# Performance work log

Measured on AMD Instinct MI355X. Metric: run time of the kernel, lower is better.

Reference implementation:

```python
import jax, jax.numpy as jnp
import numpy as np

PRIME = 2147483647  # 2^31 - 1, MinHash modulus
GAMMA = 0.3
NUM_HEADS = 8


def minhash_sketch(ids, a, b):
    # ids: (B, L, S) int64 atom ids; a,b: (K,) hash coefficients
    # h[b,l,s,k] = (a[k]*id + b[k]) mod PRIME ; signature = min over the set axis S
    h = (ids[..., None] * a + b) % PRIME          # (B, L, S, K)
    return h.min(axis=2)                          # (B, L, K)


def jaccard_from_signatures(sig_q, sig_k):
    # sig_q: (B, Lq, K), sig_k: (B, Lk, K) -> (B, Lq, Lk) fraction of matching slots.
    # Scan over the K hash slots to avoid materializing a (B,Lq,Lk,K) tensor.
    B, Lq, K = sig_q.shape
    Lk = sig_k.shape[1]

    def step(acc, cols):
        qc, kc = cols                              # (B,Lq), (B,Lk)
        return acc + (qc[:, :, None] == kc[:, None, :]).astype(jnp.float32), None

    init = jnp.zeros((B, Lq, Lk), jnp.float32)
    xs = (jnp.moveaxis(sig_q, -1, 0), jnp.moveaxis(sig_k, -1, 0))
    acc, _ = jax.lax.scan(step, init, xs)
    return acc / K


def symdiff_from_jaccard(jacc, size_q, size_k):
    # |A ∩ B| = J/(1+J) * (|A|+|B|)  =>  |A Δ B| = (|A|+|B|) * (1-J)/(1+J)
    tot = size_q[:, :, None] + size_k[:, None, :]   # (B, Lq, Lk)
    return tot * (1.0 - jacc) / (1.0 + jacc)


def setup_inputs() -> dict:
    key = jax.random.key(0)
    ks = jax.random.split(key, 12)
    B, Lq, Lk, E, S, K, V = 4, 1024, 1024, 512, 8, 128, 32000
    w = lambda k: (jax.random.normal(k, (E, E), jnp.float32) * 0.02)
    return {
        "query": jax.random.normal(ks[0], (B, Lq, E), jnp.float32),
        "key": jax.random.normal(ks[1], (B, Lk, E), jnp.float32),
        "value": jax.random.normal(ks[2], (B, Lk, E), jnp.float32),
        "token_sets_q": jax.random.randint(ks[3], (B, Lq, S), 0, V).astype(jnp.int64),
        "token_sets_k": jax.random.randint(ks[4], (B, Lk, S), 0, V).astype(jnp.int64),
        "hash_a": jax.random.randint(ks[5], (K,), 1, PRIME - 1).astype(jnp.int64),
        "hash_b": jax.random.randint(ks[6], (K,), 0, PRIME - 1).astype(jnp.int64),
        "Wq": w(ks[7]), "bq": jnp.zeros((E,), jnp.float32),
        "Wk": w(ks[8]), "bk": jnp.zeros((E,), jnp.float32),
        "Wv": w(ks[9]), "bv": jnp.zeros((E,), jnp.float32),
        "Wo": w(ks[10]), "bo": jnp.zeros((E,), jnp.float32),
    }


def reference(query, key, value, token_sets_q, token_sets_k, hash_a, hash_b,
              Wq, bq, Wk, bk, Wv, bv, Wo, bo):
    B, Lq, E = query.shape
    Lk = key.shape[1]
    H = NUM_HEADS
    d = E // H

    # in-projections (torch Linear: x @ W^T + b); q,k are computed but the
    # attention scores come solely from the token-set kernel (gating disabled)
    q = query @ Wq.T + bq
    k = key @ Wk.T + bk
    v = (value @ Wv.T + bv).reshape(B, Lk, H, d).transpose(0, 2, 1, 3)  # (B,H,Lk,d)

    # MinHash sketches of per-token atom sets -> estimated Jaccard -> Δ-RBF score
    sig_q = minhash_sketch(token_sets_q, hash_a, hash_b)   # (B,Lq,K)
    sig_k = minhash_sketch(token_sets_k, hash_a, hash_b)   # (B,Lk,K)
    jacc = jaccard_from_signatures(sig_q, sig_k)           # (B,Lq,Lk)

    S = token_sets_q.shape[-1]
    size_q = jnp.full((B, Lq), S, jnp.float32)             # uniform CSR offsets -> |set| = S
    size_k = jnp.full((B, Lk), S, jnp.float32)
    delta = symdiff_from_jaccard(jacc, size_q, size_k)
    scores = jnp.exp(-GAMMA * delta)                       # (B,Lq,Lk), shared by all heads

    attn = jax.nn.softmax(scores, axis=-1)                 # no masks, no causal, dropout=0
    ctx = jnp.einsum('bqk,bhkd->bqhd', attn, v).reshape(B, Lq, E)
    return ctx @ Wo.T + bo
```

## Files before the change

### kernel.cpp

```cpp
#include <hip/hip_runtime.h>
#include <hip/hip_bf16.h>
#include <stdint.h>

#define PRIME 2147483647u
#define GAMMA 0.3f
#define K_HASH 128
#define S_SET 8
#define NB 4
#define LQ 1024
#define LK 1024
#define EDIM 512

typedef unsigned short ushort_t;
typedef __attribute__((ext_vector_type(8))) short short8;
typedef __attribute__((ext_vector_type(4))) float f32x4;

static __device__ __forceinline__ unsigned short f2bf(float f) {
    unsigned u = __builtin_bit_cast(unsigned, f);
    u += 0x7FFFu + ((u >> 16) & 1u);
    return (unsigned short)(u >> 16);
}

static __device__ __forceinline__ void glds16(const void* g, void* l) {
    __builtin_amdgcn_global_load_lds(
        (const __attribute__((address_space(1))) unsigned int*)g,
        (__attribute__((address_space(3))) unsigned int*)l, 16, 0, 0);
}

#define SWZ(r) ((((r) >> 2) & 3) ^ ((r) & 3))

static __device__ __forceinline__ unsigned nm2(unsigned acc, unsigned a,
                                               unsigned b, unsigned ones) {
    unsigned x = a ^ b, t;
    asm("v_pk_min_u16 %0, %1, %2" : "=v"(t) : "v"(x), "v"(ones));
    return acc + t;
}
static __device__ __forceinline__ unsigned nm8(unsigned acc, int4 q, int4 k,
                                               unsigned ones) {
    acc = nm2(acc, (unsigned)q.x, (unsigned)k.x, ones);
    acc = nm2(acc, (unsigned)q.y, (unsigned)k.y, ones);
    acc = nm2(acc, (unsigned)q.z, (unsigned)k.z, ones);
    acc = nm2(acc, (unsigned)q.w, (unsigned)k.w, ones);
    return acc;
}

#define CVT_N0 (NB * LK * EDIM)
#define CVT_N1 (EDIM * EDIM)
#define CVT_N2 (EDIM * EDIM)
__global__ __launch_bounds__(256) void cvt_kernel(
        const float* __restrict__ v, const float* __restrict__ wv,
        const float* __restrict__ wo,
        ushort_t* __restrict__ vb, ushort_t* __restrict__ wvb,
        ushort_t* __restrict__ wob) {
    size_t i = ((size_t)blockIdx.x * 256 + threadIdx.x) * 8;
    const float* src; ushort_t* dst; size_t off;
    if (i < CVT_N0)                { src = v;  dst = vb;  off = i; }
    else if (i < CVT_N0 + CVT_N1)  { src = wv; dst = wvb; off = i - CVT_N0; }
    else                           { src = wo; dst = wob; off = i - CVT_N0 - CVT_N1; }
    float4 a = *(const float4*)(src + off);
    float4 b = *(const float4*)(src + off + 4);
    ushort4 o0, o1;
    o0.x = f2bf(a.x); o0.y = f2bf(a.y); o0.z = f2bf(a.z); o0.w = f2bf(a.w);
    o1.x = f2bf(b.x); o1.y = f2bf(b.y); o1.z = f2bf(b.z); o1.w = f2bf(b.w);
    *(ushort4*)(dst + off)     = o0;
    *(ushort4*)(dst + off + 4) = o1;
}

__global__ __launch_bounds__(128) void sig_kernel(
        const int* __restrict__ ts_q, const int* __restrict__ ts_k,
        const int* __restrict__ ha, const int* __restrict__ hb,
        ushort_t* __restrict__ sig_q, ushort_t* __restrict__ sig_k,
        float* __restrict__ rs) {
    int blk = blockIdx.x;
    int k = threadIdx.x;
    if (blk < 32) rs[blk * 128 + k] = 0.f;
    const int* ts = (blk < NB * LQ) ? ts_q : ts_k;
    ushort_t* sig = (blk < NB * LQ) ? sig_q : sig_k;
    int idx = blk & (NB * LQ - 1);
    unsigned long long a  = (unsigned)ha[k];
    unsigned long long bb = (unsigned)hb[k];
    __shared__ int ids[S_SET];
    if (k < S_SET) ids[k] = ts[idx * S_SET + k];
    __syncthreads();
    unsigned mn = 0xFFFFFFFFu;
    #pragma unroll
    for (int s = 0; s < S_SET; s++) {
        unsigned long long x = a * (unsigned long long)(unsigned)ids[s] + bb;
        x = (x & PRIME) + (x >> 31);
        x = (x & PRIME) + (x >> 31);
        unsigned r = (unsigned)x;
        if (r >= PRIME) r -= PRIME;
        mn = (r < mn) ? r : mn;
    }
    sig[idx * K_HASH + k] = (ushort_t)mn;
}

__global__ __launch_bounds__(256) void jaccard_kernel(
        const ushort_t* __restrict__ sig_q, const ushort_t* __restrict__ sig_k,
        ushort_t* __restrict__ P, float* __restrict__ rs) {
    __shared__ int Qs[4][128 * 16];
    __shared__ int Ks[4][64 * 17];
    __shared__ float lut[K_HASH + 1];
    int tid = threadIdx.x;
    if (tid <= K_HASH) {
        float r = (float)(K_HASH - tid) / (float)(K_HASH + tid);
        lut[tid] = expf(expf(-GAMMA * (2.0f * S_SET) * r));
    }
    int b = blockIdx.z;
    int q0 = blockIdx.y * 128, j0 = blockIdx.x * 64;
    const int4* gq = (const int4*)(sig_q + ((size_t)b * LQ + q0) * K_HASH);
    const int4* gk = (const int4*)(sig_k + ((size_t)b * LK + j0) * K_HASH);
    int r0 = tid >> 2, g0 = tid & 3;
    int r1 = 64 + r0;
    #pragma unroll
    for (int ch = 0; ch < 4; ch++) {
        *(int4*)&Qs[ch][r0 * 16 + ((g0 + (r0 >> 3)) & 3) * 4] = gq[r0 * 16 + ch * 4 + g0];
        *(int4*)&Qs[ch][r1 * 16 + ((g0 + (r1 >> 3)) & 3) * 4] = gq[r1 * 16 + ch * 4 + g0];
        *(int4*)&Ks[ch][r0 * 17 + ((g0 + (r0 >> 5)) & 3) * 4] = gk[r0 * 16 + ch * 4 + g0];
    }
    __syncthreads();
    int tx = tid & 15, ty = tid >> 4;
    unsigned ones = 0x00010001u;
    unsigned acc[8][4] = {};
    #pragma unroll 1
    for (int ch = 0; ch < 4; ch++) {
        #pragma unroll
        for (int cc = 0; cc < 4; cc++) {
            int4 qv[8], kv[4];
            #pragma unroll
            for (int i = 0; i < 8; i++)
                qv[i] = *(const int4*)&Qs[ch][(ty * 8 + i) * 16 + ((cc + ty) & 3) * 4];
            #pragma unroll
            for (int j = 0; j < 4; j++)
                kv[j] = *(const int4*)&Ks[ch][(tx * 4 + j) * 17 + ((cc + (tx >> 3)) & 3) * 4];
            #pragma unroll
            for (int i = 0; i < 8; i++)
                #pragma unroll
                for (int j = 0; j < 4; j++)
                    acc[i][j] = nm8(acc[i][j], qv[i], kv[j], ones);
        }
    }
    ushort_t* Pb = P + (size_t)b * LQ * LK;
    float fsum[8];
    #pragma unroll
    for (int i = 0; i < 8; i++) {
        ushort4 o;
        unsigned nm0 = (acc[i][0] & 0xFFFFu) + (acc[i][0] >> 16);
        unsigned nm1 = (acc[i][1] & 0xFFFFu) + (acc[i][1] >> 16);
        unsigned nm2_ = (acc[i][2] & 0xFFFFu) + (acc[i][2] >> 16);
        unsigned nm3 = (acc[i][3] & 0xFFFFu) + (acc[i][3] >> 16);
        float p0 = lut[K_HASH - nm0], p1 = lut[K_HASH - nm1];
        float p2 = lut[K_HASH - nm2_], p3 = lut[K_HASH - nm3];
        fsum[i] = (p0 + p1) + (p2 + p3);
        o.x = f2bf(p0); o.y = f2bf(p1); o.z = f2bf(p2); o.w = f2bf(p3);
        int row = q0 + ty * 8 + i;
        *(ushort4*)&Pb[(size_t)row * LK + j0 + tx * 4] = o;
    }
    __syncthreads();
    float* fs = (float*)&Qs[0][0];
    #pragma unroll
    for (int i = 0; i < 8; i++) fs[(ty * 8 + i) * 16 + tx] = fsum[i];
    __syncthreads();
    if (tid < 128) {
        float s = 0.f;
        #pragma unroll
        for (int t = 0; t < 16; t++) s += fs[tid * 16 + t];
        atomicAdd(&rs[(size_t)b * LQ + q0 + tid], s);
    }
}

#define EPI_ROWBIAS  0
#define EPI_ROWDIV   1
#define EPI_COLBIAS  2

template<int OUTF32, int MODE>
__global__ __launch_bounds__(256) void btgemm_kernel(
        const ushort_t* __restrict__ A, const ushort_t* __restrict__ B,
        void* __restrict__ C,
        const float* __restrict__ bias, const float* __restrict__ scale,
        int lda, int ldb, int ldc, int Kd,
        long long sA, long long sB, long long sC, long long sS) {
    __shared__ ushort_t As[2][64 * 32];
    __shared__ ushort_t Bs[2][64 * 32];
    int z = blockIdx.z;
    int m0 = blockIdx.y * 64, n0 = blockIdx.x * 64;
    int tid = threadIdx.x;
    int w = tid >> 6, lane = tid & 63;
    int wm = (w & 1) * 32, wn = (w >> 1) * 32;
    int mrow = lane & 15, kg = lane >> 4;

    int r = tid >> 2, c = (tid & 3) ^ SWZ(r);
    const ushort_t* pa = A + (size_t)z * sA + (size_t)(m0 + r) * lda + c * 8;
    const ushort_t* pb = B + (size_t)z * sB + (size_t)(n0 + r) * ldb + c * 8;

    int aoff[2], boff[2];
    #pragma unroll
    for (int s = 0; s < 2; s++) {
        int Ra = wm + s * 16 + mrow;
        aoff[s] = Ra * 32 + (kg ^ SWZ(Ra)) * 8;
        int Rb = wn + s * 16 + mrow;
        boff[s] = Rb * 32 + (kg ^ SWZ(Rb)) * 8;
    }

    f32x4 acc[2][2] = {};
    int nK = Kd >> 5;
    glds16(pa, &As[0][tid * 8]);
    glds16(pb, &Bs[0][tid * 8]);
    for (int i = 0; i < nK; i++) {
        __syncthreads();
        int cur = i & 1, nxt = cur ^ 1;
        if (i + 1 < nK) {
            int k0 = (i + 1) << 5;
            glds16(pa + k0, &As[nxt][tid * 8]);
            glds16(pb + k0, &Bs[nxt][tid * 8]);
        }
        short8 af[2], bh[2];
        #pragma unroll
        for (int s = 0; s < 2; s++) {
            af[s] = *(const short8*)&As[cur][aoff[s]];
            bh[s] = *(const short8*)&Bs[cur][boff[s]];
        }
        #pragma unroll
        for (int ii = 0; ii < 2; ii++)
            #pragma unroll
            for (int jj = 0; jj < 2; jj++)
                acc[ii][jj] = __builtin_amdgcn_mfma_f32_16x16x32_bf16(
                                  af[ii], bh[jj], acc[ii][jj], 0, 0, 0);
    }

    const float* sc = scale + (size_t)z * sS;
    int col = lane & 15, rbase = (lane >> 4) * 4;
    #pragma unroll
    for (int ii = 0; ii < 2; ii++) {
        #pragma unroll
        for (int jj = 0; jj < 2; jj++) {
            #pragma unroll
            for (int rr = 0; rr < 4; rr++) {
                int gm = m0 + wm + ii * 16 + rbase + rr;
                int gn = n0 + wn + jj * 16 + col;
                float v = acc[ii][jj][rr];
                if (MODE == EPI_ROWBIAS)     v += bias[gm];
                else if (MODE == EPI_ROWDIV) v /= sc[gm];
                else                         v += bias[gn];
                size_t cix = (size_t)z * sC + (size_t)gm * ldc + gn;
                if (OUTF32) ((float*)C)[cix] = v;
                else        ((ushort_t*)C)[cix] = f2bf(v);
            }
        }
    }
}

extern "C" void kernel_launch(void* const* d_in, const int* in_sizes, int n_in,
                              void* d_out, int out_size, void* d_ws, size_t ws_size,
                              hipStream_t stream) {
    const float* value = (const float*)d_in[2];
    const int* tsq = (const int*)d_in[3];
    const int* tsk = (const int*)d_in[4];
    const int* ha  = (const int*)d_in[5];
    const int* hb  = (const int*)d_in[6];
    const float* Wv = (const float*)d_in[11];
    const float* bv = (const float*)d_in[12];
    const float* Wo = (const float*)d_in[13];
    const float* bo = (const float*)d_in[14];
    float* out = (float*)d_out;

    char* ws = (char*)d_ws;
    ushort_t* sigq   = (ushort_t*)(ws);
    ushort_t* sigk   = (ushort_t*)(ws + (1ull << 20));
    ushort_t* P      = (ushort_t*)(ws + (4ull << 20));
    float* rs        = (float*)(ws + (12ull << 20));
    ushort_t* Vt     = (ushort_t*)(ws + (12ull << 20) + (1ull << 16));
    ushort_t* ctx    = (ushort_t*)(ws + (17ull << 20));
    ushort_t* Vb     = (ushort_t*)(ws + (21ull << 20));
    ushort_t* Wvb    = (ushort_t*)(ws + (25ull << 20));
    ushort_t* Wob    = (ushort_t*)(ws + (25ull << 20) + (512ull << 10));

    cvt_kernel<<<(CVT_N0 + CVT_N1 + CVT_N2) / (256 * 8), 256, 0, stream>>>(
        value, Wv, Wo, Vb, Wvb, Wob);

    sig_kernel<<<2 * NB * LQ, 128, 0, stream>>>(tsq, tsk, ha, hb, sigq, sigk, rs);

    jaccard_kernel<<<dim3(LK / 64, LQ / 128, NB), 256, 0, stream>>>(sigq, sigk, P, rs);

    btgemm_kernel<0, EPI_ROWBIAS><<<dim3(4096 / 64, 512 / 64, 1), 256, 0, stream>>>(
        Wvb, Vb, Vt, bv, rs ,
        EDIM, EDIM, NB * LK, EDIM, 0LL, 0LL, 0LL, 0LL);

    btgemm_kernel<0, EPI_ROWDIV><<<dim3(EDIM / 64, LQ / 64, NB), 256, 0, stream>>>(
        P, Vt, ctx, bv , rs,
        LK, NB * LK, EDIM, LK,
        (long long)LQ * LK, (long long)LK, (long long)LQ * EDIM, (long long)LQ);

    btgemm_kernel<1, EPI_COLBIAS><<<dim3(EDIM / 64, NB * LQ / 64, 1), 256, 0, stream>>>(
        ctx, Wob, out, bo, rs ,
        EDIM, EDIM, EDIM, EDIM, 0LL, 0LL, 0LL, 0LL);
}
```

Baseline: 156.6 us.

## Fold Wv into Wo, merge prep kernels, fuse jaccard with weight GEMM

Precomputes W2 = Wo·Wv and bias2 = Wo·bv + bo, so the value projection GEMM over all tokens is removed. The remaining pipeline is P·V followed by ctx2·W2^T, with the row division and bias folded into the final epilogue. The bf16 conversion, transpose, signature hashing and bias setup are merged into one prep kernel, and the small weight GEMM runs as extra blocks inside the jaccard kernel, whose tile shrinks to 64x64. This cuts the launch count from six to four and removes a large GEMM, at the cost of a different rounding path (bf16 W2 and unprojected V).

```diff
diff --git a/kernel.cpp b/kernel.cpp
--- a/kernel.cpp
+++ b/kernel.cpp
@@ -44,154 +44,25 @@
     return acc;
 }
 
-#define CVT_N0 (NB * LK * EDIM)
-#define CVT_N1 (EDIM * EDIM)
-#define CVT_N2 (EDIM * EDIM)
-__global__ __launch_bounds__(256) void cvt_kernel(
-        const float* __restrict__ v, const float* __restrict__ wv,
-        const float* __restrict__ wo,
-        ushort_t* __restrict__ vb, ushort_t* __restrict__ wvb,
-        ushort_t* __restrict__ wob) {
-    size_t i = ((size_t)blockIdx.x * 256 + threadIdx.x) * 8;
-    const float* src; ushort_t* dst; size_t off;
-    if (i < CVT_N0)                { src = v;  dst = vb;  off = i; }
-    else if (i < CVT_N0 + CVT_N1)  { src = wv; dst = wvb; off = i - CVT_N0; }
-    else                           { src = wo; dst = wob; off = i - CVT_N0 - CVT_N1; }
-    float4 a = *(const float4*)(src + off);
-    float4 b = *(const float4*)(src + off + 4);
-    ushort4 o0, o1;
-    o0.x = f2bf(a.x); o0.y = f2bf(a.y); o0.z = f2bf(a.z); o0.w = f2bf(a.w);
-    o1.x = f2bf(b.x); o1.y = f2bf(b.y); o1.z = f2bf(b.z); o1.w = f2bf(b.w);
-    *(ushort4*)(dst + off)     = o0;
-    *(ushort4*)(dst + off + 4) = o1;
-}
-
-__global__ __launch_bounds__(128) void sig_kernel(
-        const int* __restrict__ ts_q, const int* __restrict__ ts_k,
-        const int* __restrict__ ha, const int* __restrict__ hb,
-        ushort_t* __restrict__ sig_q, ushort_t* __restrict__ sig_k,
-        float* __restrict__ rs) {
-    int blk = blockIdx.x;
-    int k = threadIdx.x;
-    if (blk < 32) rs[blk * 128 + k] = 0.f;
-    const int* ts = (blk < NB * LQ) ? ts_q : ts_k;
-    ushort_t* sig = (blk < NB * LQ) ? sig_q : sig_k;
-    int idx = blk & (NB * LQ - 1);
-    unsigned long long a  = (unsigned)ha[k];
-    unsigned long long bb = (unsigned)hb[k];
-    __shared__ int ids[S_SET];
-    if (k < S_SET) ids[k] = ts[idx * S_SET + k];
-    __syncthreads();
-    unsigned mn = 0xFFFFFFFFu;
-    #pragma unroll
-    for (int s = 0; s < S_SET; s++) {
-        unsigned long long x = a * (unsigned long long)(unsigned)ids[s] + bb;
-        x = (x & PRIME) + (x >> 31);
-        x = (x & PRIME) + (x >> 31);
-        unsigned r = (unsigned)x;
-        if (r >= PRIME) r -= PRIME;
-        mn = (r < mn) ? r : mn;
-    }
-    sig[idx * K_HASH + k] = (ushort_t)mn;
-}
-
-__global__ __launch_bounds__(256) void jaccard_kernel(
-        const ushort_t* __restrict__ sig_q, const ushort_t* __restrict__ sig_k,
-        ushort_t* __restrict__ P, float* __restrict__ rs) {
-    __shared__ int Qs[4][128 * 16];
-    __shared__ int Ks[4][64 * 17];
-    __shared__ float lut[K_HASH + 1];
-    int tid = threadIdx.x;
-    if (tid <= K_HASH) {
-        float r = (float)(K_HASH - tid) / (float)(K_HASH + tid);
-        lut[tid] = expf(expf(-GAMMA * (2.0f * S_SET) * r));
-    }
-    int b = blockIdx.z;
-    int q0 = blockIdx.y * 128, j0 = blockIdx.x * 64;
-    const int4* gq = (const int4*)(sig_q + ((size_t)b * LQ + q0) * K_HASH);
-    const int4* gk = (const int4*)(sig_k + ((size_t)b * LK + j0) * K_HASH);
-    int r0 = tid >> 2, g0 = tid & 3;
-    int r1 = 64 + r0;
-    #pragma unroll
-    for (int ch = 0; ch < 4; ch++) {
-        *(int4*)&Qs[ch][r0 * 16 + ((g0 + (r0 >> 3)) & 3) * 4] = gq[r0 * 16 + ch * 4 + g0];
-        *(int4*)&Qs[ch][r1 * 16 + ((g0 + (r1 >> 3)) & 3) * 4] = gq[r1 * 16 + ch * 4 + g0];
-        *(int4*)&Ks[ch][r0 * 17 + ((g0 + (r0 >> 5)) & 3) * 4] = gk[r0 * 16 + ch * 4 + g0];
-    }
-    __syncthreads();
-    int tx = tid & 15, ty = tid >> 4;
-    unsigned ones = 0x00010001u;
-    unsigned acc[8][4] = {};
-    #pragma unroll 1
-    for (int ch = 0; ch < 4; ch++) {
-        #pragma unroll
-        for (int cc = 0; cc < 4; cc++) {
-            int4 qv[8], kv[4];
-            #pragma unroll
-            for (int i = 0; i < 8; i++)
-                qv[i] = *(const int4*)&Qs[ch][(ty * 8 + i) * 16 + ((cc + ty) & 3) * 4];
-            #pragma unroll
-            for (int j = 0; j < 4; j++)
-                kv[j] = *(const int4*)&Ks[ch][(tx * 4 + j) * 17 + ((cc + (tx >> 3)) & 3) * 4];
-            #pragma unroll
-            for (int i = 0; i < 8; i++)
-                #pragma unroll
-                for (int j = 0; j < 4; j++)
-                    acc[i][j] = nm8(acc[i][j], qv[i], kv[j], ones);
-        }
-    }
-    ushort_t* Pb = P + (size_t)b * LQ * LK;
-    float fsum[8];
-    #pragma unroll
-    for (int i = 0; i < 8; i++) {
-        ushort4 o;
-        unsigned nm0 = (acc[i][0] & 0xFFFFu) + (acc[i][0] >> 16);
-        unsigned nm1 = (acc[i][1] & 0xFFFFu) + (acc[i][1] >> 16);
-        unsigned nm2_ = (acc[i][2] & 0xFFFFu) + (acc[i][2] >> 16);
-        unsigned nm3 = (acc[i][3] & 0xFFFFu) + (acc[i][3] >> 16);
-        float p0 = lut[K_HASH - nm0], p1 = lut[K_HASH - nm1];
-        float p2 = lut[K_HASH - nm2_], p3 = lut[K_HASH - nm3];
-        fsum[i] = (p0 + p1) + (p2 + p3);
-        o.x = f2bf(p0); o.y = f2bf(p1); o.z = f2bf(p2); o.w = f2bf(p3);
-        int row = q0 + ty * 8 + i;
-        *(ushort4*)&Pb[(size_t)row * LK + j0 + tx * 4] = o;
-    }
-    __syncthreads();
-    float* fs = (float*)&Qs[0][0];
-    #pragma unroll
-    for (int i = 0; i < 8; i++) fs[(ty * 8 + i) * 16 + tx] = fsum[i];
-    __syncthreads();
-    if (tid < 128) {
-        float s = 0.f;
-        #pragma unroll
-        for (int t = 0; t < 16; t++) s += fs[tid * 16 + t];
-        atomicAdd(&rs[(size_t)b * LQ + q0 + tid], s);
-    }
-}
-
-#define EPI_ROWBIAS  0
-#define EPI_ROWDIV   1
-#define EPI_COLBIAS  2
+#define EPI_NONE     0
+#define EPI_DIVBIAS  1
 
 template<int OUTF32, int MODE>
-__global__ __launch_bounds__(256) void btgemm_kernel(
+static __device__ void gemm64(
         const ushort_t* __restrict__ A, const ushort_t* __restrict__ B,
         void* __restrict__ C,
         const float* __restrict__ bias, const float* __restrict__ scale,
-        int lda, int ldb, int ldc, int Kd,
-        long long sA, long long sB, long long sC, long long sS) {
-    __shared__ ushort_t As[2][64 * 32];
-    __shared__ ushort_t Bs[2][64 * 32];
-    int z = blockIdx.z;
-    int m0 = blockIdx.y * 64, n0 = blockIdx.x * 64;
-    int tid = threadIdx.x;
+        int lda, int ldb, int ldc, int Kd, int m0, int n0,
+        ushort_t* AsBase, ushort_t* BsBase, int tid) {
+    ushort_t (*As)[64 * 32] = (ushort_t (*)[64 * 32])AsBase;
+    ushort_t (*Bs)[64 * 32] = (ushort_t (*)[64 * 32])BsBase;
     int w = tid >> 6, lane = tid & 63;
     int wm = (w & 1) * 32, wn = (w >> 1) * 32;
     int mrow = lane & 15, kg = lane >> 4;
 
     int r = tid >> 2, c = (tid & 3) ^ SWZ(r);
-    const ushort_t* pa = A + (size_t)z * sA + (size_t)(m0 + r) * lda + c * 8;
-    const ushort_t* pb = B + (size_t)z * sB + (size_t)(n0 + r) * ldb + c * 8;
+    const ushort_t* pa = A + (size_t)(m0 + r) * lda + c * 8;
+    const ushort_t* pb = B + (size_t)(n0 + r) * ldb + c * 8;
 
     int aoff[2], boff[2];
     #pragma unroll
@@ -228,7 +99,6 @@
                                   af[ii], bh[jj], acc[ii][jj], 0, 0, 0);
     }
 
-    const float* sc = scale + (size_t)z * sS;
     int col = lane & 15, rbase = (lane >> 4) * 4;
     #pragma unroll
     for (int ii = 0; ii < 2; ii++) {
@@ -239,15 +109,239 @@
                 int gm = m0 + wm + ii * 16 + rbase + rr;
                 int gn = n0 + wn + jj * 16 + col;
                 float v = acc[ii][jj][rr];
-                if (MODE == EPI_ROWBIAS)     v += bias[gm];
-                else if (MODE == EPI_ROWDIV) v /= sc[gm];
-                else                         v += bias[gn];
-                size_t cix = (size_t)z * sC + (size_t)gm * ldc + gn;
+                if (MODE == EPI_DIVBIAS) v = v / scale[gm] + bias[gn];
+                size_t cix = (size_t)gm * ldc + gn;
                 if (OUTF32) ((float*)C)[cix] = v;
                 else        ((ushort_t*)C)[cix] = f2bf(v);
             }
         }
     }
+}
+
+#define PREP_WO   128
+#define PREP_TV   512
+#define PREP_TW   64
+#define PREP_SIG  1024
+#define PREP_B2   2
+#define PREP_BLOCKS (PREP_WO + PREP_TV + PREP_TW + PREP_SIG + PREP_B2)
+
+union PrepSmem {
+    ushort_t Ts[64][66];
+    float bvs[512];
+};
+
+static __device__ void tconvert(const float* __restrict__ src,
+                                ushort_t* __restrict__ dst,
+                                int R, int C, int r0, int c0, int tid,
+                                ushort_t (*Ts)[66]) {
+    int rr = tid >> 2, c4 = (tid & 3) * 16;
+    const float* s = src + (size_t)(r0 + rr) * C + c0 + c4;
+    float4 a = *(const float4*)(s + 0), b = *(const float4*)(s + 4);
+    float4 cc = *(const float4*)(s + 8), d = *(const float4*)(s + 12);
+    ushort_t* tr = &Ts[rr][c4];
+    tr[0]=f2bf(a.x);  tr[1]=f2bf(a.y);  tr[2]=f2bf(a.z);  tr[3]=f2bf(a.w);
+    tr[4]=f2bf(b.x);  tr[5]=f2bf(b.y);  tr[6]=f2bf(b.z);  tr[7]=f2bf(b.w);
+    tr[8]=f2bf(cc.x); tr[9]=f2bf(cc.y); tr[10]=f2bf(cc.z); tr[11]=f2bf(cc.w);
+    tr[12]=f2bf(d.x); tr[13]=f2bf(d.y); tr[14]=f2bf(d.z); tr[15]=f2bf(d.w);
+    __syncthreads();
+    int er = tid >> 3, bc = (tid & 7) * 8;
+    #pragma unroll
+    for (int it = 0; it < 2; it++) {
+        int e = er + it * 32;
+        ushort_t tmp[8];
+        #pragma unroll
+        for (int i = 0; i < 8; i++) tmp[i] = Ts[bc + i][e];
+        *(short8*)&dst[(size_t)(c0 + e) * R + r0 + bc] = *(const short8*)tmp;
+    }
+}
+
+__global__ __launch_bounds__(256) void prep_kernel(
+        const float* __restrict__ value, const float* __restrict__ wv,
+        const float* __restrict__ wo,
+        const float* __restrict__ bv, const float* __restrict__ bo,
+        const int* __restrict__ tsq, const int* __restrict__ tsk,
+        const int* __restrict__ ha, const int* __restrict__ hb,
+        ushort_t* __restrict__ VbT, ushort_t* __restrict__ WvT,
+        ushort_t* __restrict__ Wob,
+        ushort_t* __restrict__ sigq, ushort_t* __restrict__ sigk,
+        float* __restrict__ rs, float* __restrict__ bias2) {
+    __shared__ PrepSmem sm;
+    int blk = blockIdx.x, tid = threadIdx.x;
+    if (blk < 16) rs[blk * 256 + tid] = 0.f;
+    if (blk < PREP_WO) {
+        size_t i = ((size_t)blk * 256 + tid) * 8;
+        float4 a = *(const float4*)(wo + i), b = *(const float4*)(wo + i + 4);
+        ushort4 o0, o1;
+        o0.x=f2bf(a.x); o0.y=f2bf(a.y); o0.z=f2bf(a.z); o0.w=f2bf(a.w);
+        o1.x=f2bf(b.x); o1.y=f2bf(b.y); o1.z=f2bf(b.z); o1.w=f2bf(b.w);
+        *(ushort4*)(Wob + i)     = o0;
+        *(ushort4*)(Wob + i + 4) = o1;
+        return;
+    }
+    if (blk < PREP_WO + PREP_TV) {
+        int t = blk - PREP_WO;
+        tconvert(value, VbT, NB * LK, EDIM, (t & 63) * 64, (t >> 6) * 64, tid, sm.Ts);
+        return;
+    }
+    if (blk < PREP_WO + PREP_TV + PREP_TW) {
+        int t = blk - PREP_WO - PREP_TV;
+        tconvert(wv, WvT, EDIM, EDIM, (t & 7) * 64, (t >> 3) * 64, tid, sm.Ts);
+        return;
+    }
+    if (blk < PREP_WO + PREP_TV + PREP_TW + PREP_SIG) {
+        int sb = blk - PREP_WO - PREP_TV - PREP_TW;
+        int k = tid & 127, half = tid >> 7;
+        unsigned long long a  = (unsigned)ha[k];
+        unsigned long long bb = (unsigned)hb[k];
+        #pragma unroll
+        for (int p = 0; p < 4; p++) {
+            int row = sb * 8 + p * 2 + half;
+            const int* ts = (row < NB * LQ) ? tsq : tsk;
+            ushort_t* sig = (row < NB * LQ) ? sigq : sigk;
+            int idx = row & (NB * LQ - 1);
+            unsigned mn = 0xFFFFFFFFu;
+            #pragma unroll
+            for (int s = 0; s < S_SET; s++) {
+                unsigned long long x =
+                    a * (unsigned long long)(unsigned)ts[idx * S_SET + s] + bb;
+                x = (x & PRIME) + (x >> 31);
+                x = (x & PRIME) + (x >> 31);
+                unsigned r = (unsigned)x;
+                if (r >= PRIME) r -= PRIME;
+                mn = (r < mn) ? r : mn;
+            }
+            sig[idx * K_HASH + k] = (ushort_t)mn;
+        }
+        return;
+    }
+    int sb2 = blk - (PREP_BLOCKS - PREP_B2);
+    sm.bvs[tid] = bv[tid];
+    sm.bvs[256 + tid] = bv[256 + tid];
+    __syncthreads();
+    int n = sb2 * 256 + tid;
+    float acc = bo[n];
+    #pragma unroll 8
+    for (int e = 0; e < EDIM; e++) acc += wo[(size_t)n * EDIM + e] * sm.bvs[e];
+    bias2[n] = acc;
+}
+
+union JacwSmem {
+    struct {
+        int Qs[4][64 * 16];
+        int Ks[4][64 * 17];
+        float lut[K_HASH + 1];
+    } jac;
+    struct {
+        ushort_t As[2][64 * 32];
+        ushort_t Bs[2][64 * 32];
+    } g;
+};
+
+__global__ __launch_bounds__(256) void jacw_kernel(
+        const ushort_t* __restrict__ sigq, const ushort_t* __restrict__ sigk,
+        ushort_t* __restrict__ P, float* __restrict__ rs,
+        const ushort_t* __restrict__ Wob, const ushort_t* __restrict__ WvT,
+        ushort_t* __restrict__ W2) {
+    __shared__ JacwSmem sm;
+    int blk = blockIdx.x, tid = threadIdx.x;
+    if (blk >= 1024) {
+        int t = blk - 1024;
+        gemm64<0, EPI_NONE>(Wob, WvT, W2, nullptr, nullptr,
+                            EDIM, EDIM, EDIM, EDIM,
+                            (t >> 3) * 64, (t & 7) * 64,
+                            sm.g.As[0], sm.g.Bs[0], tid);
+        return;
+    }
+    if (tid <= K_HASH) {
+        float r = (float)(K_HASH - tid) / (float)(K_HASH + tid);
+        sm.jac.lut[tid] = expf(expf(-GAMMA * (2.0f * S_SET) * r));
+    }
+    int b = blk >> 8;
+    int q0 = ((blk >> 4) & 15) * 64, j0 = (blk & 15) * 64;
+    const int4* gq = (const int4*)(sigq + ((size_t)b * LQ + q0) * K_HASH);
+    const int4* gk = (const int4*)(sigk + ((size_t)b * LK + j0) * K_HASH);
+    int r0 = tid >> 2, g0 = tid & 3;
+    #pragma unroll
+    for (int ch = 0; ch < 4; ch++) {
+        *(int4*)&sm.jac.Qs[ch][r0 * 16 + ((g0 + (r0 >> 3)) & 3) * 4]
+            = gq[r0 * 16 + ch * 4 + g0];
+        *(int4*)&sm.jac.Ks[ch][r0 * 17 + ((g0 + (r0 >> 5)) & 3) * 4]
+            = gk[r0 * 16 + ch * 4 + g0];
+    }
+    __syncthreads();
+    int tx = tid & 15, ty = tid >> 4;
+    unsigned ones = 0x00010001u;
+    unsigned acc[4][4] = {};
+    #pragma unroll 1
+    for (int ch = 0; ch < 4; ch++) {
+        #pragma unroll
+        for (int cc = 0; cc < 4; cc++) {
+            int qo = ((cc + (ty >> 1)) & 3) * 4;
+            int ko = ((cc + (tx >> 3)) & 3) * 4;
+            int4 qv[4], kv[4];
+            #pragma unroll
+            for (int i = 0; i < 4; i++)
+                qv[i] = *(const int4*)&sm.jac.Qs[ch][(ty * 4 + i) * 16 + qo];
+            #pragma unroll
+            for (int j = 0; j < 4; j++)
+                kv[j] = *(const int4*)&sm.jac.Ks[ch][(tx * 4 + j) * 17 + ko];
+            #pragma unroll
+            for (int i = 0; i < 4; i++)
+                #pragma unroll
+                for (int j = 0; j < 4; j++)
+                    acc[i][j] = nm8(acc[i][j], qv[i], kv[j], ones);
+        }
+    }
+    ushort_t* Pb = P + (size_t)b * LQ * LK;
+    float fsum[4];
+    #pragma unroll
+    for (int i = 0; i < 4; i++) {
+        ushort4 o;
+        unsigned n0_ = (acc[i][0] & 0xFFFFu) + (acc[i][0] >> 16);
+        unsigned n1_ = (acc[i][1] & 0xFFFFu) + (acc[i][1] >> 16);
+        unsigned n2_ = (acc[i][2] & 0xFFFFu) + (acc[i][2] >> 16);
+        unsigned n3_ = (acc[i][3] & 0xFFFFu) + (acc[i][3] >> 16);
+        float p0 = sm.jac.lut[K_HASH - n0_], p1 = sm.jac.lut[K_HASH - n1_];
+        float p2 = sm.jac.lut[K_HASH - n2_], p3 = sm.jac.lut[K_HASH - n3_];
+        fsum[i] = (p0 + p1) + (p2 + p3);
+        o.x = f2bf(p0); o.y = f2bf(p1); o.z = f2bf(p2); o.w = f2bf(p3);
+        int row = q0 + ty * 4 + i;
+        *(ushort4*)&Pb[(size_t)row * LK + j0 + tx * 4] = o;
+    }
+    __syncthreads();
+    float* fs = (float*)&sm.jac.Qs[0][0];
+    #pragma unroll
+    for (int i = 0; i < 4; i++) fs[(ty * 4 + i) * 16 + tx] = fsum[i];
+    __syncthreads();
+    if (tid < 64) {
+        float s = 0.f;
+        #pragma unroll
+        for (int t = 0; t < 16; t++) s += fs[tid * 16 + t];
+        atomicAdd(&rs[(size_t)b * LQ + q0 + tid], s);
+    }
+}
+
+__global__ __launch_bounds__(256) void gemm_ctx2_kernel(
+        const ushort_t* __restrict__ P, const ushort_t* __restrict__ VbT,
+        ushort_t* __restrict__ ctx2) {
+    __shared__ ushort_t As[2][64 * 32], Bs[2][64 * 32];
+    int z = blockIdx.z;
+    gemm64<0, EPI_NONE>(P + (size_t)z * LQ * LK, VbT + (size_t)z * LK,
+                        ctx2 + (size_t)z * LQ * EDIM, nullptr, nullptr,
+                        LK, NB * LK, EDIM, LK,
+                        blockIdx.y * 64, blockIdx.x * 64,
+                        As[0], Bs[0], threadIdx.x);
+}
+
+__global__ __launch_bounds__(256) void gemm_out_kernel(
+        const ushort_t* __restrict__ ctx2, const ushort_t* __restrict__ W2,
+        float* __restrict__ out, const float* __restrict__ bias2,
+        const float* __restrict__ rs) {
+    __shared__ ushort_t As[2][64 * 32], Bs[2][64 * 32];
+    gemm64<1, EPI_DIVBIAS>(ctx2, W2, out, bias2, rs,
+                           EDIM, EDIM, EDIM, EDIM,
+                           blockIdx.y * 64, blockIdx.x * 64,
+                           As[0], Bs[0], threadIdx.x);
 }
 
 extern "C" void kernel_launch(void* const* d_in, const int* in_sizes, int n_in,
@@ -265,33 +359,25 @@
     float* out = (float*)d_out;
 
     char* ws = (char*)d_ws;
-    ushort_t* sigq   = (ushort_t*)(ws);
-    ushort_t* sigk   = (ushort_t*)(ws + (1ull << 20));
-    ushort_t* P      = (ushort_t*)(ws + (4ull << 20));
-    float* rs        = (float*)(ws + (12ull << 20));
-    ushort_t* Vt     = (ushort_t*)(ws + (12ull << 20) + (1ull << 16));
-    ushort_t* ctx    = (ushort_t*)(ws + (17ull << 20));
-    ushort_t* Vb     = (ushort_t*)(ws + (21ull << 20));
-    ushort_t* Wvb    = (ushort_t*)(ws + (25ull << 20));
-    ushort_t* Wob    = (ushort_t*)(ws + (25ull << 20) + (512ull << 10));
-
-    cvt_kernel<<<(CVT_N0 + CVT_N1 + CVT_N2) / (256 * 8), 256, 0, stream>>>(
-        value, Wv, Wo, Vb, Wvb, Wob);
-
-    sig_kernel<<<2 * NB * LQ, 128, 0, stream>>>(tsq, tsk, ha, hb, sigq, sigk, rs);
-
-    jaccard_kernel<<<dim3(LK / 64, LQ / 128, NB), 256, 0, stream>>>(sigq, sigk, P, rs);
-
-    btgemm_kernel<0, EPI_ROWBIAS><<<dim3(4096 / 64, 512 / 64, 1), 256, 0, stream>>>(
-        Wvb, Vb, Vt, bv, rs ,
-        EDIM, EDIM, NB * LK, EDIM, 0LL, 0LL, 0LL, 0LL);
-
-    btgemm_kernel<0, EPI_ROWDIV><<<dim3(EDIM / 64, LQ / 64, NB), 256, 0, stream>>>(
-        P, Vt, ctx, bv , rs,
-        LK, NB * LK, EDIM, LK,
-        (long long)LQ * LK, (long long)LK, (long long)LQ * EDIM, (long long)LQ);
-
-    btgemm_kernel<1, EPI_COLBIAS><<<dim3(EDIM / 64, NB * LQ / 64, 1), 256, 0, stream>>>(
-        ctx, Wob, out, bo, rs ,
-        EDIM, EDIM, EDIM, EDIM, 0LL, 0LL, 0LL, 0LL);
-}
+    ushort_t* sigq  = (ushort_t*)(ws);
+    ushort_t* sigk  = (ushort_t*)(ws + (1ull << 20));
+    float*    rs    = (float*)(ws + (2ull << 20));
+    float*    bias2 = (float*)(ws + (2ull << 20) + (64 << 10));
+    ushort_t* P     = (ushort_t*)(ws + (4ull << 20));
+    ushort_t* VbT   = (ushort_t*)(ws + (12ull << 20));
+    ushort_t* ctx2  = (ushort_t*)(ws + (16ull << 20));
+    ushort_t* Wob   = (ushort_t*)(ws + (20ull << 20));
+    ushort_t* WvT   = (ushort_t*)(ws + (20ull << 20) + (512 << 10));
+    ushort_t* W2    = (ushort_t*)(ws + (21ull << 20));
+
+    prep_kernel<<<PREP_BLOCKS, 256, 0, stream>>>(
+        value, Wv, Wo, bv, bo, tsq, tsk, ha, hb,
+        VbT, WvT, Wob, sigq, sigk, rs, bias2);
+
+    jacw_kernel<<<1024 + 64, 256, 0, stream>>>(sigq, sigk, P, rs, Wob, WvT, W2);
+
+    gemm_ctx2_kernel<<<dim3(EDIM / 64, LQ / 64, NB), 256, 0, stream>>>(P, VbT, ctx2);
+
+    gemm_out_kernel<<<dim3(EDIM / 64, NB * LQ / 64, 1), 256, 0, stream>>>(
+        ctx2, W2, out, bias2, rs);
+}
```

Result: slower. 168.0 us (+7.3%).
